# Optimization experiments

Measured on AMD Instinct MI355X. Metric: run time of the kernel, lower is better.

## Reference

```python
import jax, jax.numpy as jnp
import numpy as np

# SLAYER neuron / simulation constants (from netParams yaml)
THETA = 10.0      # spike threshold
TAU_SR = 10.0     # PSP (SRM) time constant, ms
TS = 1.0          # simulation time step, ms
TAU_RHO = 1.0     # surrogate-gradient width
SCALE_RHO = 1.0   # surrogate-gradient scale
N_TIME_BINS = 300 # tSample / Ts


@jax.custom_vjp
def spike_fn(u):
    # Hard threshold forward; surrogate gradient backward (SLAYER escape-rate pdf).
    return (u >= THETA).astype(u.dtype)

def _spike_fwd(u):
    return spike_fn(u), u

def _spike_bwd(u, g):
    return (g * SCALE_RHO * jnp.exp(-jnp.abs(u - THETA) / TAU_RHO),)

spike_fn.defvjp(_spike_fwd, _spike_bwd)


def psp(x):
    # Causal leaky-integrator (first-order SRM) filter over time.
    # x: [B, T, F] -> u[t] = decay * u[t-1] + x[t]
    decay = jnp.exp(jnp.asarray(-TS / TAU_SR, x.dtype))
    xT = jnp.swapaxes(x, 0, 1)  # [T, B, F]
    def step(u, xt):
        u = decay * u + xt
        return u, u
    _, out = jax.lax.scan(step, jnp.zeros_like(xT[0]), xT)
    return jnp.swapaxes(out, 0, 1)  # [B, T, F]


def rate_encode(inp, n_time_bins, key):
    # Bernoulli rate coding: spike prob per time bin = pixel intensity in [0,1].
    # inp: [B, C, H, W] -> spikes: [B, T, C*H*W]
    B = inp.shape[0]
    probs = inp.reshape(B, 1, -1)  # [B, 1, F]
    u = jax.random.uniform(key, (B, n_time_bins, probs.shape[-1]), dtype=inp.dtype)
    return (u < probs).astype(inp.dtype)


def setup_inputs() -> dict:
    key = jax.random.key(0)
    k1, k2, k3 = jax.random.split(key, 3)
    B, C, H, W = 32, 3, 32, 32
    F_in, F_hid, F_out = C * H * W, 410, 10
    inp = jax.random.uniform(k1, (B, C, H, W), dtype=jnp.float32)
    W1 = jax.random.normal(k2, (F_hid, F_in), dtype=jnp.float32) / np.sqrt(F_in).astype(np.float32)
    W2 = jax.random.normal(k3, (F_out, F_hid), dtype=jnp.float32) / np.sqrt(F_hid).astype(np.float32)
    return {"inp": inp, "W1": W1, "W2": W2}


def reference(inp, W1, W2):
    spikes = rate_encode(inp, N_TIME_BINS, jax.random.key(42))   # [B, T, 3072]
    a1 = jnp.einsum('btf,of->bto', spikes, W1)                    # dense per time bin
    s1 = spike_fn(psp(a1))                                        # [B, T, 410]
    a2 = jnp.einsum('btf,of->bto', s1, W2)
    s2 = spike_fn(psp(a2))                                        # [B, T, 10]
    return jnp.swapaxes(s2, 1, 2)                                 # [B, 10, T]
```

## Files before the change

### kernel.cpp

```cpp
#include <hip/hip_runtime.h>
#include <stdint.h>

#define B_SZ 32
#define T_SZ 300
#define F_IN 3072
#define F_HID 410
#define F_OUT 10
#define M_SZ (B_SZ * T_SZ)
#define N_PAD 448
#define KW (F_IN / 32)
#define TOTAL_ELEMS (B_SZ * T_SZ * F_IN)
#define N_WORDS (TOTAL_ELEMS / 32)
#define A2_STRIDE 16
#define NCHUNK 10
#define CLEN 30
#define NKB (F_IN / 256)
#define MT_CNT (M_SZ / 64)
#define W1_BLOCKS 672
#define RNG_BLOCKS 14400

#define DECAY 0.90483741803595957f
#define THETA 10.0f
#define KS2 (0x1BD11BDAu ^ 42u)

typedef __attribute__((ext_vector_type(8))) int i32x8;
typedef __attribute__((ext_vector_type(16))) float f32x16;

#define TF_R(r) { x0 += x1; \
  asm("v_alignbit_b32 %0, %0, %0, %1" : "+v"(x1) : "n"(32 - (r))); \
  x1 ^= x0; }

__device__ __forceinline__ uint32_t tf_bits(uint32_t x1i) {
  uint32_t x0 = 0u, x1 = x1i;
  TF_R(13) TF_R(15) TF_R(26) TF_R(6)
  x0 += 42u; x1 += KS2 + 1u;
  TF_R(17) TF_R(29) TF_R(16) TF_R(24)
  x0 += KS2; x1 += 2u;
  TF_R(13) TF_R(15) TF_R(26) TF_R(6)
  x1 += 42u + 3u;
  TF_R(17) TF_R(29) TF_R(16) TF_R(24)
  x0 += 42u; x1 += KS2 + 4u;
  TF_R(13) TF_R(15) TF_R(26) TF_R(6)
  x0 += KS2; x1 += 5u;
  return x0 ^ x1;
}

__device__ __forceinline__ void gld16(const void* g, void* l) {
  __builtin_amdgcn_global_load_lds(
      (const __attribute__((address_space(1))) uint32_t*)g,
      (__attribute__((address_space(3))) uint32_t*)l, 16, 0, 0);
}

__global__ __launch_bounds__(256) void prep(const float* __restrict__ inp,
                                            const float* __restrict__ W1,
                                            uint8_t* __restrict__ W1s,
                                            uint32_t* __restrict__ sbitsT) {
  if (blockIdx.x < W1_BLOCKS) {
    int idx = blockIdx.x * 256 + threadIdx.x;
    int g = idx * 8;
    int n = g / F_IN;
    int k = g - n * F_IN;
    uint32_t d0 = 0u, d1 = 0u;
    if (n < F_HID) {
      const float* s = W1 + (size_t)n * F_IN + k;
      float4 v0 = ((const float4*)s)[0];
      float4 v1 = ((const float4*)s)[1];
      int t0 = __builtin_amdgcn_cvt_pk_fp8_f32(v0.x, v0.y, 0, false);
      t0 = __builtin_amdgcn_cvt_pk_fp8_f32(v0.z, v0.w, t0, true);
      int t1 = __builtin_amdgcn_cvt_pk_fp8_f32(v1.x, v1.y, 0, false);
      t1 = __builtin_amdgcn_cvt_pk_fp8_f32(v1.z, v1.w, t1, true);
      d0 = (uint32_t)t0; d1 = (uint32_t)t1;
    }
    int nt = n >> 6, r = n & 63;
    int kb = k >> 8, c = (k >> 4) & 15, half = (k >> 3) & 1;
    size_t dst = ((((size_t)nt * NKB + kb) * 64 + r) * 16 + (c ^ (r & 15))) * 16 + half * 8;
    *(uint2*)(W1s + dst) = make_uint2(d0, d1);
  } else {
    uint32_t idx = (blockIdx.x - W1_BLOCKS) * 256u + threadIdx.x;
    uint32_t q = idx & 3u;
    uint32_t j = idx >> 2;
    uint32_t r = j & 63u;
    uint32_t t1 = j >> 6;
    uint32_t wi = t1 & 7u;
    uint32_t t2 = t1 >> 3;
    uint32_t kb = t2 % (uint32_t)NKB;
    uint32_t mt = t2 / (uint32_t)NKB;
    uint32_t m = mt * 64u + r;
    uint32_t b = m / (uint32_t)T_SZ;
    uint32_t f = (kb * 8u + wi) * 32u + q * 8u;
    const float* p = inp + b * F_IN + f;
    float4 va = ((const float4*)p)[0];
    float4 vb = ((const float4*)p)[1];
    uint32_t T0 = (uint32_t)ceilf(va.x * 8388608.0f);
    uint32_t T1 = (uint32_t)ceilf(va.y * 8388608.0f);
    uint32_t T2 = (uint32_t)ceilf(va.z * 8388608.0f);
    uint32_t T3 = (uint32_t)ceilf(va.w * 8388608.0f);
    uint32_t T4 = (uint32_t)ceilf(vb.x * 8388608.0f);
    uint32_t T5 = (uint32_t)ceilf(vb.y * 8388608.0f);
    uint32_t T6 = (uint32_t)ceilf(vb.z * 8388608.0f);
    uint32_t T7 = (uint32_t)ceilf(vb.w * 8388608.0f);
    uint32_t b42 = m * (uint32_t)F_IN + f + 42u;
    uint32_t w = 0u;
#define GEN(jj, Tn) { uint32_t bits = tf_bits(b42 + (jj)); \
  w |= ((bits >> 9) < (Tn)) ? (1u << (jj)) : 0u; }
    GEN(0, T0) GEN(1, T1) GEN(2, T2) GEN(3, T3)
    GEN(4, T4) GEN(5, T5) GEN(6, T6) GEN(7, T7)
#undef GEN
    ((uint8_t*)sbitsT)[idx] = (uint8_t)w;
  }
}

__global__ __launch_bounds__(256) void gemm1(const uint32_t* __restrict__ sbitsT,
                                             const uint8_t* __restrict__ W1s,
                                             float* __restrict__ a1) {
  __shared__ uint32_t sAT[2][8 * 64];
  __shared__ uint8_t sB[2][64 * 256];

  const int tid = threadIdx.x;
  const int mtile = blockIdx.x;
  const int nt = blockIdx.y;
  const int m0 = mtile * 64;
  const int n0 = nt * 64;
  const int wv = tid >> 6, lane = tid & 63;
  const int wm = (wv & 1) * 32, wn = (wv >> 1) * 32;
  const int l31 = lane & 31, lh = lane >> 5;

  const uint8_t* gB0 = W1s + (size_t)nt * NKB * 16384;
  const uint8_t* gA0 = (const uint8_t*)sbitsT + (size_t)mtile * NKB * 2048;

  auto STAGE = [&](int buf, int kb) {
    const uint8_t* gB = gB0 + (size_t)kb * 16384;
#pragma unroll
    for (int q = 0; q < 4; ++q)
      gld16(gB + (wv * 4 + q) * 1024 + lane * 16, &sB[buf][(wv * 4 + q) * 1024]);
    if (wv < 2)
      gld16(gA0 + (size_t)kb * 2048 + wv * 1024 + lane * 16,
            (uint8_t*)&sAT[buf][0] + wv * 1024);
  };

  f32x16 acc;
#pragma unroll
  for (int e = 0; e < 16; ++e) acc[e] = 0.0f;

  STAGE(0, 0);
  __syncthreads();
  int cur = 0;
  for (int kb = 0; kb < NKB; ++kb) {
    if (kb + 1 < NKB) STAGE(cur ^ 1, kb + 1);
    const uint8_t* sBc = sB[cur];
    const uint32_t* sATc = sAT[cur];
#pragma unroll
    for (int sub = 0; sub < 4; ++sub) {
      int row = wn + l31;
      int cb = sub * 4 + lh * 2;
      uint4 u0 = *(uint4*)&sBc[row * 256 + (((cb + 0) ^ (row & 15)) << 4)];
      uint4 u1 = *(uint4*)&sBc[row * 256 + (((cb + 1) ^ (row & 15)) << 4)];
      i32x8 bfr;
      bfr[0] = u0.x; bfr[1] = u0.y; bfr[2] = u0.z; bfr[3] = u0.w;
      bfr[4] = u1.x; bfr[5] = u1.y; bfr[6] = u1.z; bfr[7] = u1.w;
      uint32_t w = sATc[(sub * 2 + lh) * 64 + wm + l31];
      i32x8 afr;
#pragma unroll
      for (int j = 0; j < 8; ++j) {
        uint32_t n = (w >> (4 * j)) & 15u;
        afr[j] = (int)(((n * 0x204081u) & 0x01010101u) * 0x38u);
      }
      acc = __builtin_amdgcn_mfma_scale_f32_32x32x64_f8f6f4(
          afr, bfr, acc, 0, 0, 0, 127, 0, 127);
    }
    __syncthreads();
    cur ^= 1;
  }
  int col = n0 + wn + l31;
#pragma unroll
  for (int rg = 0; rg < 16; ++rg) {
    int row = m0 + wm + (rg & 3) + 8 * (rg >> 2) + 4 * lh;
    a1[(size_t)row * N_PAD + col] = acc[rg];
  }
}

__global__ __launch_bounds__(256) void psp1_partial(float* __restrict__ a1,
                                                    float* __restrict__ fin) {
  int idx = blockIdx.x * 256 + threadIdx.x;
  if (idx >= B_SZ * NCHUNK * N_PAD) return;
  int o = idx % N_PAD;
  int bc = idx / N_PAD;
  int c = bc % NCHUNK;
  int b = bc / NCHUNK;
  float* p = a1 + ((size_t)(b * T_SZ + c * CLEN)) * N_PAD + o;
  float u = 0.0f;
#pragma unroll
  for (int i = 0; i < CLEN; ++i) {
    u = __fadd_rn(__fmul_rn(DECAY, u), p[(size_t)i * N_PAD]);
    p[(size_t)i * N_PAD] = u;
  }
  fin[(size_t)bc * N_PAD + o] = u;
}

__global__ __launch_bounds__(256) void fscan(float* __restrict__ fin) {
  int idx = blockIdx.x * 256 + threadIdx.x;
  if (idx >= B_SZ * N_PAD) return;
  int o = idx % N_PAD;
  int b = idx / N_PAD;
  float* f = fin + (size_t)b * NCHUNK * N_PAD + o;
  float d30 = 1.0f;
#pragma unroll
  for (int i = 0; i < CLEN; ++i) d30 *= DECAY;
  float v[NCHUNK - 1];
#pragma unroll
  for (int c = 0; c < NCHUNK - 1; ++c) v[c] = f[(size_t)c * N_PAD];
  float F = 0.0f;
  f[0] = 0.0f;
#pragma unroll
  for (int c = 1; c < NCHUNK; ++c) {
    F = v[c - 1] + d30 * F;
    f[(size_t)c * N_PAD] = F;
  }
}

__global__ __launch_bounds__(256) void apply_gemm2(const float* __restrict__ a1,
                                                   const float* __restrict__ fin,
                                                   const float* __restrict__ W2,
                                                   float* __restrict__ a2) {
  __shared__ float sW2[F_OUT * F_HID];
  for (int i = threadIdx.x; i < F_OUT * F_HID; i += 256) sW2[i] = W2[i];
  __syncthreads();
  int m = blockIdx.x * 4 + (threadIdx.x >> 6);
  int lane = threadIdx.x & 63;
  int b = m / T_SZ, t = m % T_SZ;
  int c = t / CLEN, tl = t % CLEN;
  float dp = DECAY;
  for (int i = 0; i < tl; ++i) dp *= DECAY;
  const float* frow = fin + (size_t)(b * NCHUNK + c) * N_PAD;
  float p[F_OUT];
#pragma unroll
  for (int o = 0; o < F_OUT; ++o) p[o] = 0.0f;
#pragma unroll
  for (int j = 0; j < 7; ++j) {
    int hh = lane + j * 64;
    float u = a1[(size_t)m * N_PAD + hh];
    if (c > 0) {
      float F = frow[hh];
      u = __fadd_rn(u, __fmul_rn(dp, F));
    }
    bool valid = hh < F_HID;
    float s = (u >= THETA && valid) ? 1.0f : 0.0f;
    int hcl = valid ? hh : 0;
#pragma unroll
    for (int o = 0; o < F_OUT; ++o) p[o] = fmaf(s, sW2[o * F_HID + hcl], p[o]);
  }
#pragma unroll
  for (int o = 0; o < F_OUT; ++o)
#pragma unroll
    for (int s = 1; s < 64; s <<= 1) p[o] += __shfl_xor(p[o], s, 64);
  if (lane < F_OUT) a2[(size_t)m * A2_STRIDE + lane] = p[lane];
}

__global__ __launch_bounds__(128) void psp2(const float* __restrict__ a2,
                                            float* __restrict__ out) {
  __shared__ float chf[NCHUNK][F_OUT];
  __shared__ float seed[NCHUNK][F_OUT];
  int b = blockIdx.x;
  int tid = threadIdx.x;
  int o = tid / NCHUNK, c = tid % NCHUNK;
  const float* p = a2 + ((size_t)(b * T_SZ + c * CLEN)) * A2_STRIDE + o;
  float v[CLEN];
  float pa[CLEN];
  if (tid < F_OUT * NCHUNK) {
#pragma unroll
    for (int i = 0; i < CLEN; ++i) v[i] = p[(size_t)i * A2_STRIDE];
    float u = 0.0f;
#pragma unroll
    for (int i = 0; i < CLEN; ++i) {
      u = __fadd_rn(__fmul_rn(DECAY, u), v[i]);
      pa[i] = u;
    }
    chf[c][o] = u;
  }
  __syncthreads();
  if (tid < F_OUT) {
    float d30 = 1.0f;
#pragma unroll
    for (int i = 0; i < CLEN; ++i) d30 *= DECAY;
    float F = 0.0f;
    for (int cc = 0; cc < NCHUNK; ++cc) {
      F = chf[cc][tid] + d30 * F;
      seed[cc][tid] = F;
    }
  }
  __syncthreads();
  if (tid < F_OUT * NCHUNK) {
    float F = (c == 0) ? 0.0f : seed[c - 1][o];
    float dp = DECAY;
    float* q = out + (size_t)b * F_OUT * T_SZ + (size_t)o * T_SZ + c * CLEN;
#pragma unroll
    for (int i = 0; i < CLEN; ++i) {
      float u = (c == 0) ? pa[i] : __fadd_rn(pa[i], __fmul_rn(dp, F));
      q[i] = (u >= THETA) ? 1.0f : 0.0f;
      dp *= DECAY;
    }
  }
}

extern "C" void kernel_launch(void* const* d_in, const int* in_sizes, int n_in,
                              void* d_out, int out_size, void* d_ws, size_t ws_size,
                              hipStream_t stream) {
  const float* inp = (const float*)d_in[0];
  const float* W1  = (const float*)d_in[1];
  const float* W2  = (const float*)d_in[2];
  float* out = (float*)d_out;
  char* ws = (char*)d_ws;
  uint8_t* W1s = (uint8_t*)(ws);
  uint32_t* sbitsT = (uint32_t*)(ws + 1376256);
  float* a1 = (float*)(ws + 1376256 + 3686400);
  float* fin = a1 + (size_t)M_SZ * N_PAD;
  float* a2 = fin + (size_t)B_SZ * NCHUNK * N_PAD;

  prep<<<dim3(W1_BLOCKS + RNG_BLOCKS), dim3(256), 0, stream>>>(inp, W1, W1s, sbitsT);
  gemm1<<<dim3(MT_CNT, N_PAD / 64), dim3(256), 0, stream>>>(sbitsT, W1s, a1);
  psp1_partial<<<dim3((B_SZ * NCHUNK * N_PAD) / 256), dim3(256), 0, stream>>>(a1, fin);
  fscan<<<dim3((B_SZ * N_PAD) / 256), dim3(256), 0, stream>>>(fin);
  apply_gemm2<<<dim3(M_SZ / 4), dim3(256), 0, stream>>>(a1, fin, W2, a2);
  psp2<<<dim3(B_SZ), dim3(128), 0, stream>>>(a2, out);
}
```

Measured before the change: 165.6 us.

## Fuse prep and gemm1 into persistent kernel with per-mtile dependency counters

Replaces the separate prep (W1 fp8 conversion and RNG spike-bit generation) and gemm1 launches with one persistent kernel that walks a tick schedule. RNG work for later m-tiles is interleaved with GEMM tiles for earlier ones, and atomic counters gate each GEMM tile on its W1 and spike-bit inputs. The goal is to overlap the ALU-heavy Threefry generation with the MFMA work and to remove one launch boundary. In exchange it adds spin-waiting, fences, an extra tiny zeroing kernel, and relies on all persistent blocks being co-resident to avoid deadlock.

```diff
diff --git a/kernel.cpp b/kernel.cpp
--- a/kernel.cpp
+++ b/kernel.cpp
@@ -8,16 +8,18 @@
 #define F_OUT 10
 #define M_SZ (B_SZ * T_SZ)
 #define N_PAD 448
-#define KW (F_IN / 32)
-#define TOTAL_ELEMS (B_SZ * T_SZ * F_IN)
-#define N_WORDS (TOTAL_ELEMS / 32)
 #define A2_STRIDE 16
 #define NCHUNK 10
 #define CLEN 30
 #define NKB (F_IN / 256)
 #define MT_CNT (M_SZ / 64)
-#define W1_BLOCKS 672
-#define RNG_BLOCKS 14400
+#define W1_UNITS 672
+#define RNG_UNITS 14400
+
+#define TK_RNG0 672
+#define TK_GRP 864
+#define TK_TAIL (TK_GRP + 148 * 103)
+#define NTICK (TK_TAIL + 14)
 
 #define DECAY 0.90483741803595957f
 #define THETA 10.0f
@@ -51,74 +53,80 @@
       (__attribute__((address_space(3))) uint32_t*)l, 16, 0, 0);
 }
 
-__global__ __launch_bounds__(256) void prep(const float* __restrict__ inp,
-                                            const float* __restrict__ W1,
-                                            uint8_t* __restrict__ W1s,
-                                            uint32_t* __restrict__ sbitsT) {
-  if (blockIdx.x < W1_BLOCKS) {
-    int idx = blockIdx.x * 256 + threadIdx.x;
-    int g = idx * 8;
-    int n = g / F_IN;
-    int k = g - n * F_IN;
-    uint32_t d0 = 0u, d1 = 0u;
-    if (n < F_HID) {
-      const float* s = W1 + (size_t)n * F_IN + k;
-      float4 v0 = ((const float4*)s)[0];
-      float4 v1 = ((const float4*)s)[1];
-      int t0 = __builtin_amdgcn_cvt_pk_fp8_f32(v0.x, v0.y, 0, false);
-      t0 = __builtin_amdgcn_cvt_pk_fp8_f32(v0.z, v0.w, t0, true);
-      int t1 = __builtin_amdgcn_cvt_pk_fp8_f32(v1.x, v1.y, 0, false);
-      t1 = __builtin_amdgcn_cvt_pk_fp8_f32(v1.z, v1.w, t1, true);
-      d0 = (uint32_t)t0; d1 = (uint32_t)t1;
-    }
-    int nt = n >> 6, r = n & 63;
-    int kb = k >> 8, c = (k >> 4) & 15, half = (k >> 3) & 1;
-    size_t dst = ((((size_t)nt * NKB + kb) * 64 + r) * 16 + (c ^ (r & 15))) * 16 + half * 8;
-    *(uint2*)(W1s + dst) = make_uint2(d0, d1);
-  } else {
-    uint32_t idx = (blockIdx.x - W1_BLOCKS) * 256u + threadIdx.x;
-    uint32_t q = idx & 3u;
-    uint32_t j = idx >> 2;
-    uint32_t r = j & 63u;
-    uint32_t t1 = j >> 6;
-    uint32_t wi = t1 & 7u;
-    uint32_t t2 = t1 >> 3;
-    uint32_t kb = t2 % (uint32_t)NKB;
-    uint32_t mt = t2 / (uint32_t)NKB;
-    uint32_t m = mt * 64u + r;
-    uint32_t b = m / (uint32_t)T_SZ;
-    uint32_t f = (kb * 8u + wi) * 32u + q * 8u;
-    const float* p = inp + b * F_IN + f;
-    float4 va = ((const float4*)p)[0];
-    float4 vb = ((const float4*)p)[1];
-    uint32_t T0 = (uint32_t)ceilf(va.x * 8388608.0f);
-    uint32_t T1 = (uint32_t)ceilf(va.y * 8388608.0f);
-    uint32_t T2 = (uint32_t)ceilf(va.z * 8388608.0f);
-    uint32_t T3 = (uint32_t)ceilf(va.w * 8388608.0f);
-    uint32_t T4 = (uint32_t)ceilf(vb.x * 8388608.0f);
-    uint32_t T5 = (uint32_t)ceilf(vb.y * 8388608.0f);
-    uint32_t T6 = (uint32_t)ceilf(vb.z * 8388608.0f);
-    uint32_t T7 = (uint32_t)ceilf(vb.w * 8388608.0f);
-    uint32_t b42 = m * (uint32_t)F_IN + f + 42u;
-    uint32_t w = 0u;
+__device__ __forceinline__ uint32_t* ctr_slot(uint32_t* ctr, int i) {
+  return ctr + (size_t)i * A2_STRIDE + 10;
+}
+
+__global__ __launch_bounds__(256) void zeroctr(uint32_t* __restrict__ ctr) {
+  if (threadIdx.x < 152) *ctr_slot(ctr, threadIdx.x) = 0u;
+}
+
+
+__device__ __forceinline__ void w1_unit(int u, int tid,
+                                        const float* __restrict__ W1,
+                                        uint8_t* __restrict__ W1s) {
+  int idx = u * 256 + tid;
+  int g = idx * 8;
+  int n = g / F_IN;
+  int k = g - n * F_IN;
+  uint32_t d0 = 0u, d1 = 0u;
+  if (n < F_HID) {
+    const float* s = W1 + (size_t)n * F_IN + k;
+    float4 v0 = ((const float4*)s)[0];
+    float4 v1 = ((const float4*)s)[1];
+    int t0 = __builtin_amdgcn_cvt_pk_fp8_f32(v0.x, v0.y, 0, false);
+    t0 = __builtin_amdgcn_cvt_pk_fp8_f32(v0.z, v0.w, t0, true);
+    int t1 = __builtin_amdgcn_cvt_pk_fp8_f32(v1.x, v1.y, 0, false);
+    t1 = __builtin_amdgcn_cvt_pk_fp8_f32(v1.z, v1.w, t1, true);
+    d0 = (uint32_t)t0; d1 = (uint32_t)t1;
+  }
+  int nt = n >> 6, r = n & 63;
+  int kb = k >> 8, c = (k >> 4) & 15, half = (k >> 3) & 1;
+  size_t dst = ((((size_t)nt * NKB + kb) * 64 + r) * 16 + (c ^ (r & 15))) * 16 + half * 8;
+  *(uint2*)(W1s + dst) = make_uint2(d0, d1);
+}
+
+__device__ __forceinline__ void rng_unit(int bp, int tid,
+                                         const float* __restrict__ inp,
+                                         uint32_t* __restrict__ sbitsT) {
+  uint32_t idx = (uint32_t)bp * 256u + tid;
+  uint32_t q = idx & 3u;
+  uint32_t j = idx >> 2;
+  uint32_t r = j & 63u;
+  uint32_t t1 = j >> 6;
+  uint32_t wi = t1 & 7u;
+  uint32_t t2 = t1 >> 3;
+  uint32_t kb = t2 % (uint32_t)NKB;
+  uint32_t mt = t2 / (uint32_t)NKB;
+  uint32_t m = mt * 64u + r;
+  uint32_t b = m / (uint32_t)T_SZ;
+  uint32_t f = (kb * 8u + wi) * 32u + q * 8u;
+  const float* p = inp + b * F_IN + f;
+  float4 va = ((const float4*)p)[0];
+  float4 vb = ((const float4*)p)[1];
+  uint32_t T0 = (uint32_t)ceilf(va.x * 8388608.0f);
+  uint32_t T1 = (uint32_t)ceilf(va.y * 8388608.0f);
+  uint32_t T2 = (uint32_t)ceilf(va.z * 8388608.0f);
+  uint32_t T3 = (uint32_t)ceilf(va.w * 8388608.0f);
+  uint32_t T4 = (uint32_t)ceilf(vb.x * 8388608.0f);
+  uint32_t T5 = (uint32_t)ceilf(vb.y * 8388608.0f);
+  uint32_t T6 = (uint32_t)ceilf(vb.z * 8388608.0f);
+  uint32_t T7 = (uint32_t)ceilf(vb.w * 8388608.0f);
+  uint32_t b42 = m * (uint32_t)F_IN + f + 42u;
+  uint32_t w = 0u;
 #define GEN(jj, Tn) { uint32_t bits = tf_bits(b42 + (jj)); \
   w |= ((bits >> 9) < (Tn)) ? (1u << (jj)) : 0u; }
-    GEN(0, T0) GEN(1, T1) GEN(2, T2) GEN(3, T3)
-    GEN(4, T4) GEN(5, T5) GEN(6, T6) GEN(7, T7)
+  GEN(0, T0) GEN(1, T1) GEN(2, T2) GEN(3, T3)
+  GEN(4, T4) GEN(5, T5) GEN(6, T6) GEN(7, T7)
 #undef GEN
-    ((uint8_t*)sbitsT)[idx] = (uint8_t)w;
-  }
-}
-
-__global__ __launch_bounds__(256) void gemm1(const uint32_t* __restrict__ sbitsT,
-                                             const uint8_t* __restrict__ W1s,
-                                             float* __restrict__ a1) {
-  __shared__ uint32_t sAT[2][8 * 64];
-  __shared__ uint8_t sB[2][64 * 256];
-
-  const int tid = threadIdx.x;
-  const int mtile = blockIdx.x;
-  const int nt = blockIdx.y;
+  ((uint8_t*)sbitsT)[idx] = (uint8_t)w;
+}
+
+__device__ __forceinline__ void gemm_unit(int mtile, int nt, int tid,
+                                          const uint32_t* __restrict__ sbitsT,
+                                          const uint8_t* __restrict__ W1s,
+                                          float* __restrict__ a1,
+                                          uint32_t* sAT, uint8_t* sB) {
   const int m0 = mtile * 64;
   const int n0 = nt * 64;
   const int wv = tid >> 6, lane = tid & 63;
@@ -132,10 +140,11 @@
     const uint8_t* gB = gB0 + (size_t)kb * 16384;
 #pragma unroll
     for (int q = 0; q < 4; ++q)
-      gld16(gB + (wv * 4 + q) * 1024 + lane * 16, &sB[buf][(wv * 4 + q) * 1024]);
+      gld16(gB + (wv * 4 + q) * 1024 + lane * 16,
+            sB + buf * 16384 + (wv * 4 + q) * 1024);
     if (wv < 2)
       gld16(gA0 + (size_t)kb * 2048 + wv * 1024 + lane * 16,
-            (uint8_t*)&sAT[buf][0] + wv * 1024);
+            (uint8_t*)sAT + buf * 2048 + wv * 1024);
   };
 
   f32x16 acc;
@@ -147,8 +156,8 @@
   int cur = 0;
   for (int kb = 0; kb < NKB; ++kb) {
     if (kb + 1 < NKB) STAGE(cur ^ 1, kb + 1);
-    const uint8_t* sBc = sB[cur];
-    const uint32_t* sATc = sAT[cur];
+    const uint8_t* sBc = sB + cur * 16384;
+    const uint32_t* sATc = sAT + cur * 512;
 #pragma unroll
     for (int sub = 0; sub < 4; ++sub) {
       int row = wn + l31;
@@ -176,6 +185,55 @@
   for (int rg = 0; rg < 16; ++rg) {
     int row = m0 + wm + (rg & 3) + 8 * (rg >> 2) + 4 * lh;
     a1[(size_t)row * N_PAD + col] = acc[rg];
+  }
+}
+
+__global__ __launch_bounds__(256, 4) void rnggemm(
+    const float* __restrict__ inp, const float* __restrict__ W1,
+    uint8_t* __restrict__ W1s, uint32_t* __restrict__ sbitsT,
+    float* __restrict__ a1, uint32_t* __restrict__ ctr) {
+  __shared__ uint32_t sAT[2 * 512];
+  __shared__ uint8_t sB[2 * 16384];
+  const int tid = threadIdx.x;
+  const int G = gridDim.x;
+  for (int T = blockIdx.x; T < NTICK; T += G) {
+    if (T < W1_UNITS) {
+      w1_unit(T, tid, W1, W1s);
+      __syncthreads();
+      if (tid == 0) { __threadfence(); atomicAdd(ctr_slot(ctr, 1), 1u); }
+    } else {
+      int x = T - TK_RNG0;
+      int bp = -1, mtile = 0, nt = 0;
+      if (x < 192) {
+        bp = x;
+      } else {
+        x -= 192;
+        if (T < TK_TAIL) {
+          int g = x / 103, r = x - g * 103;
+          if (r < 96) bp = (g + 2) * 96 + r;
+          else { mtile = g; nt = r - 96; }
+        } else {
+          int y = T - TK_TAIL;
+          mtile = 148 + y / 7; nt = y - (y / 7) * 7;
+        }
+      }
+      if (bp >= 0) {
+        rng_unit(bp, tid, inp, sbitsT);
+        __syncthreads();
+        if (tid == 0) { __threadfence(); atomicAdd(ctr_slot(ctr, 2 + bp / 96), 1u); }
+      } else {
+        if (tid == 0) {
+          while (__hip_atomic_load(ctr_slot(ctr, 1), __ATOMIC_RELAXED,
+                                   __HIP_MEMORY_SCOPE_AGENT) < (uint32_t)W1_UNITS ||
+                 __hip_atomic_load(ctr_slot(ctr, 2 + mtile), __ATOMIC_RELAXED,
+                                   __HIP_MEMORY_SCOPE_AGENT) < 96u)
+            __builtin_amdgcn_s_sleep(2);
+          __threadfence();
+        }
+        __syncthreads();
+        gemm_unit(mtile, nt, tid, sbitsT, W1s, a1, sAT, sB);
+      }
+    }
   }
 }
 
@@ -315,9 +373,19 @@
   float* a1 = (float*)(ws + 1376256 + 3686400);
   float* fin = a1 + (size_t)M_SZ * N_PAD;
   float* a2 = fin + (size_t)B_SZ * NCHUNK * N_PAD;
-
-  prep<<<dim3(W1_BLOCKS + RNG_BLOCKS), dim3(256), 0, stream>>>(inp, W1, W1s, sbitsT);
-  gemm1<<<dim3(MT_CNT, N_PAD / 64), dim3(256), 0, stream>>>(sbitsT, W1s, a1);
+  uint32_t* ctr = (uint32_t*)a2;
+
+  static int NBLK = 0;
+  if (NBLK == 0) {
+    int t = 0;
+    if (hipOccupancyMaxActiveBlocksPerMultiprocessor(&t, rnggemm, 256, 0) != hipSuccess || t < 1)
+      t = 1;
+    if (t > 4) t = 4;
+    NBLK = t * 256;
+  }
+
+  zeroctr<<<dim3(1), dim3(256), 0, stream>>>(ctr);
+  rnggemm<<<dim3(NBLK), dim3(256), 0, stream>>>(inp, W1, W1s, sbitsT, a1, ctr);
   psp1_partial<<<dim3((B_SZ * NCHUNK * N_PAD) / 256), dim3(256), 0, stream>>>(a1, fin);
   fscan<<<dim3((B_SZ * N_PAD) / 256), dim3(256), 0, stream>>>(fin);
   apply_gemm2<<<dim3(M_SZ / 4), dim3(256), 0, stream>>>(a1, fin, W2, a2);
```

Measured after the change: 559.2 us. +237.7%, slower.

## Fuse layer-1 PSP scan and thresholding into one kernel emitting spike bitmasks

Applied to the files above, without the earlier changes.

Replaces the partial-scan, carry-scan and apply kernels with a single kernel that reads a1 once, resolves chunk carries via shared memory, and writes ballot-packed spike bits. The second GEMM then reads compact bitmasks instead of float potentials and chunk carries. This removes the a1 write-back and re-read plus a launch, at the cost of a small grid of large blocks with low occupancy.

```diff
diff --git a/kernel.cpp b/kernel.cpp
--- a/kernel.cpp
+++ b/kernel.cpp
@@ -8,10 +8,8 @@
 #define F_OUT 10
 #define M_SZ (B_SZ * T_SZ)
 #define N_PAD 448
-#define KW (F_IN / 32)
-#define TOTAL_ELEMS (B_SZ * T_SZ * F_IN)
-#define N_WORDS (TOTAL_ELEMS / 32)
 #define A2_STRIDE 16
+#define SB2_STRIDE 16
 #define NCHUNK 10
 #define CLEN 30
 #define NKB (F_IN / 256)
@@ -179,73 +177,61 @@
   }
 }
 
-__global__ __launch_bounds__(256) void psp1_partial(float* __restrict__ a1,
-                                                    float* __restrict__ fin) {
-  int idx = blockIdx.x * 256 + threadIdx.x;
-  if (idx >= B_SZ * NCHUNK * N_PAD) return;
-  int o = idx % N_PAD;
-  int bc = idx / N_PAD;
-  int c = bc % NCHUNK;
-  int b = bc / NCHUNK;
-  float* p = a1 + ((size_t)(b * T_SZ + c * CLEN)) * N_PAD + o;
+__global__ __launch_bounds__(640) void scan_spike(const float* __restrict__ a1,
+                                                  uint32_t* __restrict__ sb2) {
+  __shared__ float fin_s[NCHUNK][64];
+  const int oblk = blockIdx.x;
+  const int b = blockIdx.y;
+  const int c = threadIdx.x >> 6;
+  const int lane = threadIdx.x & 63;
+  const int o = oblk * 64 + lane;
+  const float* p = a1 + ((size_t)(b * T_SZ + c * CLEN)) * N_PAD + o;
+  float pa[CLEN];
   float u = 0.0f;
 #pragma unroll
   for (int i = 0; i < CLEN; ++i) {
     u = __fadd_rn(__fmul_rn(DECAY, u), p[(size_t)i * N_PAD]);
-    p[(size_t)i * N_PAD] = u;
-  }
-  fin[(size_t)bc * N_PAD + o] = u;
-}
-
-__global__ __launch_bounds__(256) void fscan(float* __restrict__ fin) {
-  int idx = blockIdx.x * 256 + threadIdx.x;
-  if (idx >= B_SZ * N_PAD) return;
-  int o = idx % N_PAD;
-  int b = idx / N_PAD;
-  float* f = fin + (size_t)b * NCHUNK * N_PAD + o;
+    pa[i] = u;
+  }
+  fin_s[c][lane] = u;
+  __syncthreads();
   float d30 = 1.0f;
 #pragma unroll
   for (int i = 0; i < CLEN; ++i) d30 *= DECAY;
-  float v[NCHUNK - 1];
-#pragma unroll
-  for (int c = 0; c < NCHUNK - 1; ++c) v[c] = f[(size_t)c * N_PAD];
   float F = 0.0f;
-  f[0] = 0.0f;
-#pragma unroll
-  for (int c = 1; c < NCHUNK; ++c) {
-    F = v[c - 1] + d30 * F;
-    f[(size_t)c * N_PAD] = F;
-  }
-}
-
-__global__ __launch_bounds__(256) void apply_gemm2(const float* __restrict__ a1,
-                                                   const float* __restrict__ fin,
-                                                   const float* __restrict__ W2,
-                                                   float* __restrict__ a2) {
+  for (int cc = 0; cc < c; ++cc)
+    F = fin_s[cc][lane] + d30 * F;
+  float dp = DECAY;
+  const int m0 = b * T_SZ + c * CLEN;
+#pragma unroll
+  for (int i = 0; i < CLEN; ++i) {
+    float uu = (c > 0) ? __fadd_rn(pa[i], __fmul_rn(dp, F)) : pa[i];
+    unsigned long long msk = __ballot(uu >= THETA);
+    if (lane == 0)
+      *(uint2*)&sb2[(size_t)(m0 + i) * SB2_STRIDE + oblk * 2] =
+          make_uint2((uint32_t)msk, (uint32_t)(msk >> 32));
+    dp *= DECAY;
+  }
+}
+
+__global__ __launch_bounds__(256) void gemm2(const uint32_t* __restrict__ sb2,
+                                             const float* __restrict__ W2,
+                                             float* __restrict__ a2) {
   __shared__ float sW2[F_OUT * F_HID];
   for (int i = threadIdx.x; i < F_OUT * F_HID; i += 256) sW2[i] = W2[i];
   __syncthreads();
   int m = blockIdx.x * 4 + (threadIdx.x >> 6);
   int lane = threadIdx.x & 63;
-  int b = m / T_SZ, t = m % T_SZ;
-  int c = t / CLEN, tl = t % CLEN;
-  float dp = DECAY;
-  for (int i = 0; i < tl; ++i) dp *= DECAY;
-  const float* frow = fin + (size_t)(b * NCHUNK + c) * N_PAD;
+  int lh = lane >> 5;
   float p[F_OUT];
 #pragma unroll
   for (int o = 0; o < F_OUT; ++o) p[o] = 0.0f;
 #pragma unroll
   for (int j = 0; j < 7; ++j) {
     int hh = lane + j * 64;
-    float u = a1[(size_t)m * N_PAD + hh];
-    if (c > 0) {
-      float F = frow[hh];
-      u = __fadd_rn(u, __fmul_rn(dp, F));
-    }
-    bool valid = hh < F_HID;
-    float s = (u >= THETA && valid) ? 1.0f : 0.0f;
-    int hcl = valid ? hh : 0;
+    uint32_t w = sb2[(size_t)m * SB2_STRIDE + j * 2 + lh];
+    float s = (float)((w >> (lane & 31)) & 1u);
+    int hcl = hh < F_HID ? hh : 0;
 #pragma unroll
     for (int o = 0; o < F_OUT; ++o) p[o] = fmaf(s, sW2[o * F_HID + hcl], p[o]);
   }
@@ -313,13 +299,12 @@
   uint8_t* W1s = (uint8_t*)(ws);
   uint32_t* sbitsT = (uint32_t*)(ws + 1376256);
   float* a1 = (float*)(ws + 1376256 + 3686400);
-  float* fin = a1 + (size_t)M_SZ * N_PAD;
-  float* a2 = fin + (size_t)B_SZ * NCHUNK * N_PAD;
+  uint32_t* sb2 = (uint32_t*)((char*)a1 + (size_t)M_SZ * N_PAD * 4);
+  float* a2 = (float*)((char*)sb2 + (size_t)M_SZ * SB2_STRIDE * 4);
 
   prep<<<dim3(W1_BLOCKS + RNG_BLOCKS), dim3(256), 0, stream>>>(inp, W1, W1s, sbitsT);
   gemm1<<<dim3(MT_CNT, N_PAD / 64), dim3(256), 0, stream>>>(sbitsT, W1s, a1);
-  psp1_partial<<<dim3((B_SZ * NCHUNK * N_PAD) / 256), dim3(256), 0, stream>>>(a1, fin);
-  fscan<<<dim3((B_SZ * N_PAD) / 256), dim3(256), 0, stream>>>(fin);
-  apply_gemm2<<<dim3(M_SZ / 4), dim3(256), 0, stream>>>(a1, fin, W2, a2);
+  scan_spike<<<dim3(N_PAD / 64, B_SZ), dim3(640), 0, stream>>>(a1, sb2);
+  gemm2<<<dim3(M_SZ / 4), dim3(256), 0, stream>>>(sb2, W2, a2);
   psp2<<<dim3(B_SZ), dim3(128), 0, stream>>>(a2, out);
 }
```

Measured after the change: 161.0 us. 2.7% less time.
